# Kernel tuning notes

Hardware: AMD Instinct MI355X
Metric: run time of the kernel (lower is better)

## Reference

```python
import jax, jax.numpy as jnp
import numpy as np


def _prelu(x, a):
    # nn.PReLU() with a single learnable parameter a
    return jnp.where(x >= 0, x, a * x)


def _conv1x1(x, w, b):
    # x: [n, cin, h, w], w: [cout, cin], b: [cout]
    return jnp.einsum('nchw,oc->nohw', x, w) + b[None, :, None, None]


def setup_inputs() -> dict:
    key = jax.random.key(0)
    ks = jax.random.split(key, 7)
    N, C, H, W = 8, 64, 64, 64
    red = 2
    c = C // red
    s = 1.0 / np.sqrt(C).astype(np.float32)
    x = jax.random.normal(ks[0], (N, C, H, W), dtype=jnp.float32)
    w1 = jax.random.normal(ks[1], (c, C), dtype=jnp.float32) * s
    b1 = jnp.zeros((c,), dtype=jnp.float32)
    w2 = jax.random.normal(ks[2], (c, C), dtype=jnp.float32) * s
    b2 = jnp.zeros((c,), dtype=jnp.float32)
    w3 = jax.random.normal(ks[3], (C, C), dtype=jnp.float32) * s
    b3 = jnp.zeros((C,), dtype=jnp.float32)
    a1 = jnp.full((1,), 0.25, dtype=jnp.float32)
    a2 = jnp.full((1,), 0.25, dtype=jnp.float32)
    a3 = jnp.full((1,), 0.25, dtype=jnp.float32)
    return {"x": x, "w1": w1, "b1": b1, "a1": a1, "w2": w2, "b2": b2,
            "a2": a2, "w3": w3, "b3": b3, "a3": a3}


def reference(x, w1, b1, a1, w2, b2, a2, w3, b3, a3):
    res_scale = 1.0
    n, C, h, w = x.shape
    e1 = _prelu(_conv1x1(x, w1, b1), a1[0])  # [n, c, h, w]
    e2 = _prelu(_conv1x1(x, w2, b2), a2[0])  # [n, c, h, w]
    e3 = _prelu(_conv1x1(x, w3, b3), a3[0])  # [n, C, h, w]
    c = e1.shape[1]
    hw = h * w
    q = e1.transpose(0, 2, 3, 1).reshape(n, hw, c)   # [n, hw, c]
    k = e2.reshape(n, c, hw)                         # [n, c, hw]
    score = jax.nn.softmax(jnp.matmul(q, k), axis=-1)  # [n, hw, hw]
    v = e3.reshape(n, C, hw).transpose(0, 2, 1)      # [n, hw, C]
    out = jnp.matmul(score, v)                       # [n, hw, C]
    out = out.transpose(0, 2, 1).reshape(n, C, h, w)
    return out + res_scale * x
```

## Files before the change

kernel.cpp:

```cpp
#include <hip/hip_runtime.h>
#include <hip/hip_bf16.h>

typedef __bf16 bf16x8 __attribute__((ext_vector_type(8)));
typedef float  f32x4  __attribute__((ext_vector_type(4)));
typedef float  f32x16 __attribute__((ext_vector_type(16)));
typedef int    i32x4  __attribute__((ext_vector_type(4)));

#define SEQ 4096
#define CIN 64
#define KBLK 64
#define KSPLIT 4
#define KCHUNK (SEQ / KSPLIT)
#define NTC (KCHUNK / KBLK)
#define LOG2E 1.44269504088896340736f

__device__ __forceinline__ void gll16(const void* g, void* l) {
    __builtin_amdgcn_global_load_lds(
        (const __attribute__((address_space(1))) void*)g,
        (__attribute__((address_space(3))) void*)l, 16, 0, 0);
}

__device__ __forceinline__ unsigned cvtpk(float lo, float hi) {
    unsigned r;
    asm("v_cvt_pk_bf16_f32 %0, %1, %2" : "=v"(r) : "v"(lo), "v"(hi));
    return r;
}

__global__ __launch_bounds__(256, 2) void qkv_gen(
    const float* __restrict__ x,
    const float* __restrict__ w1, const float* __restrict__ b1, const float* __restrict__ a1,
    const float* __restrict__ w2, const float* __restrict__ b2, const float* __restrict__ a2,
    const float* __restrict__ w3, const float* __restrict__ b3, const float* __restrict__ a3,
    __bf16* __restrict__ qws, __bf16* __restrict__ kws, __bf16* __restrict__ vtws)
{
    __shared__ float xs[CIN][64];
    __shared__ float wl[CIN][128];
    __shared__ float bl[128];
    __shared__ float al[4];

    const int t  = threadIdx.x;
    const int n  = blockIdx.x >> 6;
    const int p0 = (blockIdx.x & 63) << 6;

    for (int idx = t; idx < 2048; idx += 256) {
        int j = idx >> 6, c = idx & 63;
        wl[c][j]      = w1[idx];
        wl[c][32 + j] = w2[idx];
    }
    for (int idx = t; idx < 4096; idx += 256) {
        int j = idx >> 6, c = idx & 63;
        wl[c][64 + j] = w3[idx];
    }
    if (t < 32) { bl[t] = b1[t]; bl[32 + t] = b2[t]; }
    if (t >= 128 && t < 192) bl[64 + (t - 128)] = b3[t - 128];
    if (t == 0) { al[0] = a1[0]; al[1] = a2[0]; al[2] = a3[0]; }

    const float* xb = x + ((size_t)n * CIN) * SEQ + p0;
    for (int r = 0; r < 16; ++r) {
        int e = r * 256 + t;
        xs[e >> 6][e & 63] = xb[(size_t)(e >> 6) * SEQ + (e & 63)];
    }
    __syncthreads();

    const int p  = t & 63;
    const int g  = t >> 6;
    const int jb = g << 5;
    const float a = (g == 0) ? al[0] : ((g == 1) ? al[1] : al[2]);

    float acc[32];
    #pragma unroll
    for (int j = 0; j < 32; ++j) acc[j] = bl[jb + j];

    for (int c = 0; c < CIN; ++c) {
        float xv = xs[c][p];
        const f32x4* wr = (const f32x4*)&wl[c][jb];
        #pragma unroll
        for (int j4 = 0; j4 < 8; ++j4) {
            f32x4 wv = wr[j4];
            acc[j4*4+0] = fmaf(wv[0], xv, acc[j4*4+0]);
            acc[j4*4+1] = fmaf(wv[1], xv, acc[j4*4+1]);
            acc[j4*4+2] = fmaf(wv[2], xv, acc[j4*4+2]);
            acc[j4*4+3] = fmaf(wv[3], xv, acc[j4*4+3]);
        }
    }
    #pragma unroll
    for (int j = 0; j < 32; ++j) acc[j] = acc[j] >= 0.f ? acc[j] : a * acc[j];

    const int pg = p0 + p;
    if (g <= 1) {
        const float sc = (g == 0) ? LOG2E : 1.0f;
        __bf16* dst = (g == 0 ? qws : kws) + ((size_t)n * SEQ + pg) * 32;
        #pragma unroll
        for (int v8 = 0; v8 < 4; ++v8) {
            bf16x8 o;
            #pragma unroll
            for (int i = 0; i < 8; ++i) o[i] = (__bf16)(acc[v8*8+i] * sc);
            *(bf16x8*)(dst + v8*8) = o;
        }
    } else {
        __bf16* dst = vtws + ((size_t)n * CIN + (jb - 64)) * SEQ + pg;
        #pragma unroll
        for (int j = 0; j < 32; ++j) dst[(size_t)j * SEQ] = (__bf16)acc[j];
    }
}

__global__ __launch_bounds__(256) void attn(
    const __bf16* __restrict__ qws, const __bf16* __restrict__ kws,
    const __bf16* __restrict__ vtws,
    float* __restrict__ Ows, float* __restrict__ lws)
{
    __shared__ __align__(16) char ktl[2][KBLK * 64];
    __shared__ __align__(16) char vtl[2][CIN * KBLK*2];

    const int t    = threadIdx.x;
    const int lane = t & 63;
    const int wid  = t >> 6;
    const int n    = blockIdx.x & 7;
    const int qblk = (blockIdx.x >> 3) & 31;
    const int ks   = blockIdx.x >> 8;
    const int l31  = lane & 31;
    const int h    = lane >> 5;
    const int qbase = qblk * 128 + wid * 32;
    const int kbase = ks * KCHUNK;
    const int ksw  = ((l31 >> 1) & 3) << 4;
    const int vsw  = (l31 & 7) << 4;

    const char* kb = (const char*)(kws + (size_t)n * SEQ * 32);
    const char* vb = (const char*)(vtws + (size_t)n * CIN * SEQ);

    const char* qp = (const char*)(qws + (size_t)n * SEQ * 32)
                     + (size_t)(qbase + l31) * 64 + h * 16;
    const bf16x8 qf0 = *(const bf16x8*)(qp);
    const bf16x8 qf1 = *(const bf16x8*)(qp + 32);

    f32x16 of0 = {}, of1 = {};
    float ls = 0.f;

    auto stage = [&](int k0n, int buf) {
        {
            int row = t >> 2;
            int c16 = (t & 3) ^ ((t >> 3) & 3);
            gll16(kb + (size_t)(k0n + row) * 64 + c16 * 16, &ktl[buf][0] + t * 16);
        }
        #pragma unroll
        for (int j = 0; j < 2; ++j) {
            int L   = j * 4096 + t * 16;
            int row = j * 32 + (t >> 3);
            int c16 = (t & 7) ^ ((t >> 3) & 7);
            gll16(vb + (size_t)row * 8192 + (size_t)k0n * 2 + c16 * 16, &vtl[buf][0] + L);
        }
    };

    stage(kbase, 0);
    __syncthreads();

    for (int tt = 0; tt < NTC; ++tt) {
        const int cur = tt & 1;
        if (tt + 1 < NTC) stage(kbase + (tt + 1) * KBLK, cur ^ 1);

        const char* kc_ = &ktl[cur][0];
        const char* vc_ = &vtl[cur][0];

        unsigned c0[8], c1[8];

        #pragma unroll
        for (int kti = 0; kti < 2; ++kti) {
            const char* krow = kc_ + (size_t)(kti * 32 + l31) * 64;
            bf16x8 kf0 = *(const bf16x8*)(krow + ((h * 16) ^ ksw));
            bf16x8 kf1 = *(const bf16x8*)(krow + ((32 + h * 16) ^ ksw));
            f32x16 s = {};
            __builtin_amdgcn_s_setprio(1);
            s = __builtin_amdgcn_mfma_f32_32x32x16_bf16(kf0, qf0, s, 0, 0, 0);
            s = __builtin_amdgcn_mfma_f32_32x32x16_bf16(kf1, qf1, s, 0, 0, 0);
            __builtin_amdgcn_s_setprio(0);

            float p[16];
            #pragma unroll
            for (int r = 0; r < 16; ++r) {
                p[r] = __builtin_exp2f(s[r]);
                ls += p[r];
            }
            unsigned* c = kti ? c1 : c0;
            #pragma unroll
            for (int j = 0; j < 4; ++j) {
                c[j]     = cvtpk(p[2*j],     p[2*j + 1]);
                c[4 + j] = cvtpk(p[8 + 2*j], p[9 + 2*j]);
            }
            asm("v_permlane32_swap_b32 %0, %1" : "+v"(c[0]), "+v"(c[2]));
            asm("v_permlane32_swap_b32 %0, %1" : "+v"(c[1]), "+v"(c[3]));
            asm("v_permlane32_swap_b32 %0, %1" : "+v"(c[4]), "+v"(c[6]));
            asm("v_permlane32_swap_b32 %0, %1" : "+v"(c[5]), "+v"(c[7]));
        }

        __builtin_amdgcn_s_setprio(1);
        #pragma unroll
        for (int s4 = 0; s4 < 4; ++s4) {
            const unsigned* cs = (s4 < 2) ? c0 : c1;
            const int sl = (s4 & 1) * 4;
            i32x4 bi = { (int)cs[sl], (int)cs[sl+1], (int)cs[sl+2], (int)cs[sl+3] };
            bf16x8 pf = __builtin_bit_cast(bf16x8, bi);
            const int colv = (s4 * 32 + h * 16) ^ vsw;
            bf16x8 vf0 = *(const bf16x8*)(vc_ + (size_t)l31 * 128 + colv);
            bf16x8 vf1 = *(const bf16x8*)(vc_ + (size_t)(32 + l31) * 128 + colv);
            of0 = __builtin_amdgcn_mfma_f32_32x32x16_bf16(vf0, pf, of0, 0, 0, 0);
            of1 = __builtin_amdgcn_mfma_f32_32x32x16_bf16(vf1, pf, of1, 0, 0, 0);
        }
        __builtin_amdgcn_s_setprio(0);

        __syncthreads();
    }

    const int qg = qbase + l31;
    float* Ob = Ows + (size_t)n * CIN * SEQ;
    #pragma unroll
    for (int r = 0; r < 16; ++r) {
        int dv = (r & 3) + 8 * (r >> 2) + 4 * h;
        unsafeAtomicAdd(Ob + (size_t)dv * SEQ + qg,        of0[r]);
        unsafeAtomicAdd(Ob + (size_t)(dv + 32) * SEQ + qg, of1[r]);
    }
    unsafeAtomicAdd(lws + n * SEQ + qg, ls);
}

__global__ __launch_bounds__(256) void combine(
    const float* __restrict__ Ows, const float* __restrict__ lws,
    const float* __restrict__ x, float* __restrict__ out)
{
    const int total = 8 * CIN * SEQ / 4;
    for (int i = blockIdx.x * 256 + threadIdx.x; i < total; i += gridDim.x * 256) {
        int q4 = i & (SEQ / 4 - 1);
        int nd = i >> 10;
        int n  = nd >> 6;
        f32x4 o4 = *(const f32x4*)(Ows + (size_t)i * 4);
        f32x4 l4 = *(const f32x4*)(lws + (size_t)n * SEQ + q4 * 4);
        f32x4 x4 = *(const f32x4*)(x + (size_t)i * 4);
        f32x4 r;
        r[0] = o4[0] / l4[0] + x4[0];
        r[1] = o4[1] / l4[1] + x4[1];
        r[2] = o4[2] / l4[2] + x4[2];
        r[3] = o4[3] / l4[3] + x4[3];
        *(f32x4*)(out + (size_t)i * 4) = r;
    }
}

extern "C" void kernel_launch(void* const* d_in, const int* in_sizes, int n_in,
                              void* d_out, int out_size, void* d_ws, size_t ws_size,
                              hipStream_t stream)
{
    (void)in_sizes; (void)n_in; (void)out_size; (void)ws_size;
    const float* x  = (const float*)d_in[0];
    const float* w1 = (const float*)d_in[1];
    const float* b1 = (const float*)d_in[2];
    const float* a1 = (const float*)d_in[3];
    const float* w2 = (const float*)d_in[4];
    const float* b2 = (const float*)d_in[5];
    const float* a2 = (const float*)d_in[6];
    const float* w3 = (const float*)d_in[7];
    const float* b3 = (const float*)d_in[8];
    const float* a3 = (const float*)d_in[9];
    float* out = (float*)d_out;

    char* ws = (char*)d_ws;
    __bf16* qws  = (__bf16*)(ws);
    __bf16* kws  = (__bf16*)(ws + (2u << 20));
    __bf16* vtws = (__bf16*)(ws + (4u << 20));
    float*  Ows  = (float*)(ws + (8u << 20));
    float*  lws  = (float*)(ws + (16u << 20));

    hipMemsetAsync(Ows, 0, (8u << 20) + (128u << 10), stream);
    hipLaunchKernelGGL(qkv_gen, dim3(512), dim3(256), 0, stream,
                       x, w1, b1, a1, w2, b2, a2, w3, b3, a3, qws, kws, vtws);
    hipLaunchKernelGGL(attn, dim3(8 * 32 * KSPLIT), dim3(256), 0, stream,
                       qws, kws, vtws, Ows, lws);
    hipLaunchKernelGGL(combine, dim3(1024), dim3(256), 0, stream,
                       Ows, lws, x, out);
}
```

Baseline: 99.57 us.

## Triple-buffer K/V staging with vmcnt waits and single barrier per tile

Replaces the double-buffered K/V LDS staging with a three-stage ring buffer that prefetches two tiles ahead. Explicit s_waitcnt vmcnt counts plus one s_barrier per iteration replace the two __syncthreads, so global loads can overlap more compute. It also adds an occupancy hint to launch_bounds. LDS use grows to 36KB per block, which may limit occupancy, and the hand-set vmcnt counts depend on the exact number of loads issued per stage.

```diff
diff --git a/kernel.cpp b/kernel.cpp
--- a/kernel.cpp
+++ b/kernel.cpp
@@ -104,20 +104,19 @@
     }
 }
 
-__global__ __launch_bounds__(256) void attn(
+__global__ __launch_bounds__(256, 4) void attn(
     const __bf16* __restrict__ qws, const __bf16* __restrict__ kws,
     const __bf16* __restrict__ vtws,
     float* __restrict__ Ows, float* __restrict__ lws)
 {
-    __shared__ __align__(16) char ktl[2][KBLK * 64];
-    __shared__ __align__(16) char vtl[2][CIN * KBLK*2];
+    __shared__ __align__(16) char stg[3][12288];
 
     const int t    = threadIdx.x;
     const int lane = t & 63;
-    const int wid  = t >> 6;
     const int n    = blockIdx.x & 7;
     const int qblk = (blockIdx.x >> 3) & 31;
     const int ks   = blockIdx.x >> 8;
+    const int wid  = t >> 6;
     const int l31  = lane & 31;
     const int h    = lane >> 5;
     const int qbase = qblk * 128 + wid * 32;
@@ -136,30 +135,41 @@
     f32x16 of0 = {}, of1 = {};
     float ls = 0.f;
 
-    auto stage = [&](int k0n, int buf) {
+    auto stage = [&](int k0n, int b) {
         {
             int row = t >> 2;
             int c16 = (t & 3) ^ ((t >> 3) & 3);
-            gll16(kb + (size_t)(k0n + row) * 64 + c16 * 16, &ktl[buf][0] + t * 16);
+            gll16(kb + (size_t)(k0n + row) * 64 + c16 * 16, &stg[b][0] + t * 16);
         }
         #pragma unroll
         for (int j = 0; j < 2; ++j) {
             int L   = j * 4096 + t * 16;
             int row = j * 32 + (t >> 3);
             int c16 = (t & 7) ^ ((t >> 3) & 7);
-            gll16(vb + (size_t)row * 8192 + (size_t)k0n * 2 + c16 * 16, &vtl[buf][0] + L);
+            gll16(vb + (size_t)row * 8192 + (size_t)k0n * 2 + c16 * 16,
+                  &stg[b][4096] + L);
         }
     };
 
     stage(kbase, 0);
-    __syncthreads();
-
+    stage(kbase + KBLK, 1);
+
+    int cur = 0;
     for (int tt = 0; tt < NTC; ++tt) {
-        const int cur = tt & 1;
-        if (tt + 1 < NTC) stage(kbase + (tt + 1) * KBLK, cur ^ 1);
-
-        const char* kc_ = &ktl[cur][0];
-        const char* vc_ = &vtl[cur][0];
+        if (tt + 1 < NTC) {
+            asm volatile("s_waitcnt vmcnt(3)" ::: "memory");
+        } else {
+            asm volatile("s_waitcnt vmcnt(0)" ::: "memory");
+        }
+        __builtin_amdgcn_s_barrier();
+
+        if (tt + 2 < NTC) {
+            int nb = cur + 2; if (nb >= 3) nb -= 3;
+            stage(kbase + (tt + 2) * KBLK, nb);
+        }
+
+        const char* kc_ = &stg[cur][0];
+        const char* vc_ = &stg[cur][4096];
 
         unsigned c0[8], c1[8];
 
@@ -207,7 +217,7 @@
         }
         __builtin_amdgcn_s_setprio(0);
 
-        __syncthreads();
+        cur = (cur == 2) ? 0 : cur + 1;
     }
 
     const int qg = qbase + l31;
```

After: 90.94 us. 1.09x faster.
